# Optimization experiments

Measured on AMD Instinct MI355X. Metric: run time of the kernel, lower is better.

The kernel has to match this reference:

```python
import jax, jax.numpy as jnp
import numpy as np

B, T, E = 2, 4096, 768
H = 12
WIN = 256  # one-sided window w; band width = 2w+1


def setup_inputs() -> dict:
    key = jax.random.key(0)
    k1, k2, k3, k4 = jax.random.split(key, 4)
    scale = 1.0 / np.sqrt(E)
    return {
        "x": jax.random.normal(k1, (B, T, E), dtype=jnp.float32),
        "Wq": jax.random.normal(k2, (E, E), dtype=jnp.float32) * scale,
        "Wk": jax.random.normal(k3, (E, E), dtype=jnp.float32) * scale,
        "Wv": jax.random.normal(k4, (E, E), dtype=jnp.float32) * scale,
    }


def reference(x, Wq, Wk, Wv):
    b, t, e = x.shape
    h, w = H, WIN
    s = e // h
    Wb = 2 * w + 1          # band width
    nc = t // w             # number of query chunks of size w

    # projections (nn.Linear, bias=False): y = x @ W^T
    q = (x @ Wq.T).reshape(b, t, h, s) * (1.0 / np.sqrt(s))
    k = (x @ Wk.T).reshape(b, t, h, s)
    v = (x @ Wv.T).reshape(b, t, h, s)

    # overlapping key/value chunks: chunk c covers absolute keys [c*w - w, c*w + 2w)
    pad = [(0, 0), (w, w), (0, 0), (0, 0)]
    kp = jnp.pad(k, pad).reshape(b, nc + 2, w, h, s)
    k3 = jnp.concatenate([kp[:, :-2], kp[:, 1:-1], kp[:, 2:]], axis=2)  # [b,nc,3w,h,s]
    vp = jnp.pad(v, pad).reshape(b, nc + 2, w, h, s)
    v3 = jnp.concatenate([vp[:, :-2], vp[:, 1:-1], vp[:, 2:]], axis=2)  # [b,nc,3w,h,s]

    qc = q.reshape(b, nc, w, h, s)
    scores = jnp.einsum('bcxhd,bcyhd->bhcxy', qc, k3)  # [b,h,nc,w,3w]

    # extract the banded diagonals: band j <-> key index p + j in the 3w window
    idx = jnp.arange(w)[:, None] + jnp.arange(Wb)[None, :]  # [w, 2w+1], values in [0,3w)
    band = jnp.take_along_axis(scores, idx[None, None, None], axis=-1)  # [b,h,nc,w,2w+1]
    band = band.reshape(b, h, t, Wb).transpose(0, 2, 1, 3)  # [b,t,h,2w+1]

    # mask_invalid_locations: key absolute pos = i + j - w must lie in [0, t)
    key_pos = jnp.arange(t)[:, None] + jnp.arange(Wb)[None, :] - w
    invalid = (key_pos < 0) | (key_pos >= t)
    band = jnp.where(invalid[None, :, None, :], -jnp.inf, band)

    probs = jax.nn.softmax(band.astype(jnp.float32), axis=-1).astype(x.dtype)

    # sliding_chunks_matmul_pv: scatter band probs back to the 3w window layout
    pc = probs.transpose(0, 2, 1, 3).reshape(b, h, nc, w, Wb)
    pc_pad = jnp.pad(pc, [(0, 0)] * 4 + [(w - 1, w - 1)])  # last axis len 4w-1
    # full[p, m] = band[p, m - p] for m-p in [0, 2w], else 0
    idx2 = (jnp.arange(3 * w)[None, :] - jnp.arange(w)[:, None]) + (w - 1)  # [w, 3w]
    pfull = jnp.take_along_axis(pc_pad, idx2[None, None, None], axis=-1)  # [b,h,nc,w,3w]

    out = jnp.einsum('bhcpm,bcmhd->bcphd', pfull, v3).reshape(b, t, e)
    return out
```

## Files before the change

kernel.cpp:

```cpp
#include <hip/hip_runtime.h>

#define B_ 2
#define T_ 4096
#define E_ 768
#define H_ 12
#define S_ 64
#define WIN_ 256
#define GX_ 32
#define TP_ 4128

typedef unsigned short u16;
typedef unsigned int u32;
typedef __attribute__((ext_vector_type(8))) short bf16x8;
typedef __attribute__((ext_vector_type(4))) short bf16x4;
typedef __attribute__((ext_vector_type(4))) float f32x4;

__device__ __forceinline__ u16 f2bf(float f) {
  u32 u = __float_as_uint(f);
  u += ((u >> 16) & 1u) + 0x7fffu;
  return (u16)(u >> 16);
}

__device__ __forceinline__ u32 cvt_pk_bf16(float lo, float hi) {
  u32 r;
  asm("v_cvt_pk_bf16_f32 %0, %1, %2" : "=v"(r) : "v"(lo), "v"(hi));
  return r;
}

__device__ __forceinline__ void async_copy16(const u16* g, u16* l) {
  __builtin_amdgcn_global_load_lds(
      (const __attribute__((address_space(1))) void*)g,
      (__attribute__((address_space(3))) void*)l, 16, 0, 0);
}

__global__ void cvt_all(const float* __restrict__ x, const float* __restrict__ wq,
                        const float* __restrict__ wk, const float* __restrict__ wv,
                        u16* __restrict__ xb, u16* __restrict__ wb) {
  const int n4x = B_ * T_ * E_ / 4;
  const int n4w = E_ * E_ / 4;
  int i = blockIdx.x * 256 + threadIdx.x;
  const float* src;
  u16* dst;
  int j;
  if (i < n4x) {
    src = x; dst = xb; j = i;
  } else {
    int t = i - n4x;
    int z = t / n4w;
    if (z >= 3) return;
    j = t - z * n4w;
    src = (z == 0) ? wq : ((z == 1) ? wk : wv);
    dst = wb + (size_t)z * E_ * E_;
  }
  float4 v = ((const float4*)src)[j];
  ushort4 o;
  o.x = f2bf(v.x); o.y = f2bf(v.y); o.z = f2bf(v.z); o.w = f2bf(v.w);
  ((ushort4*)dst)[j] = o;
}

__global__ __launch_bounds__(256)
void gemm_qkv(const u16* __restrict__ xb, const u16* __restrict__ wb,
              u16* __restrict__ qkv) {
  const int M = B_ * T_;
  __shared__ u16 As[3][128][32];
  __shared__ u16 Bs[3][128][32];
  int tid = threadIdx.x;
  int lane = tid & 63, wave = tid >> 6;
  int wr = wave >> 1, wc = wave & 1;
  int q8 = lane >> 4, nl = lane & 15;
  int bm = blockIdx.x * 128, bn = blockIdx.y * 128;
  int z = blockIdx.z;
  const u16* A = xb;
  const u16* Bmat = wb + (size_t)z * E_ * E_;
  u16* C = qkv + (size_t)z * M * E_;
  float scale = (z == 0) ? (0.125f * 1.44269504088896f) : 1.0f;

  int r0 = tid >> 2, c0 = tid & 3;
  int cs = c0 ^ (r0 & 3);
  const u16* ga0 = A + (size_t)(bm + r0) * E_ + cs * 8;
  const u16* ga1 = A + (size_t)(bm + r0 + 64) * E_ + cs * 8;
  const u16* gb0 = Bmat + (size_t)(bn + r0) * E_ + cs * 8;
  const u16* gb1 = Bmat + (size_t)(bn + r0 + 64) * E_ + cs * 8;
  int l0 = tid * 8;
  int l1 = tid * 8 + 2048;

  int swz8 = (q8 ^ (nl & 3)) * 8;

  const int NK = E_ / 32;
#pragma unroll
  for (int p = 0; p < 2; ++p) {
    int koff = p * 32;
    async_copy16(ga0 + koff, &As[p][0][0] + l0);
    async_copy16(ga1 + koff, &As[p][0][0] + l1);
    async_copy16(gb0 + koff, &Bs[p][0][0] + l0);
    async_copy16(gb1 + koff, &Bs[p][0][0] + l1);
  }

  f32x4 acc[4][4] = {};

#define KSTEP(KI, BUF, PBUF)                                                   \
  {                                                                            \
    asm volatile("s_waitcnt vmcnt(4) lgkmcnt(0)" ::: "memory");                \
    __builtin_amdgcn_s_barrier();                                              \
    __builtin_amdgcn_sched_barrier(0);                                         \
    int kp = ((KI) + 2 < NK) ? (KI) + 2 : NK - 1;                              \
    int koff = kp * 32;                                                        \
    async_copy16(ga0 + koff, &As[PBUF][0][0] + l0);                            \
    async_copy16(ga1 + koff, &As[PBUF][0][0] + l1);                            \
    async_copy16(gb0 + koff, &Bs[PBUF][0][0] + l0);                            \
    async_copy16(gb1 + koff, &Bs[PBUF][0][0] + l1);                            \
    bf16x8 af[4], bfr[4];                                                      \
    _Pragma("unroll")                                                          \
    for (int i = 0; i < 4; ++i)                                                \
      af[i] = *(const bf16x8*)&As[BUF][wr * 64 + i * 16 + nl][swz8];           \
    _Pragma("unroll")                                                          \
    for (int i = 0; i < 4; ++i)                                                \
      bfr[i] = *(const bf16x8*)&Bs[BUF][wc * 64 + i * 16 + nl][swz8];          \
    __builtin_amdgcn_s_setprio(1);                                             \
    _Pragma("unroll")                                                          \
    for (int i = 0; i < 4; ++i)                                                \
      _Pragma("unroll")                                                        \
      for (int j2 = 0; j2 < 4; ++j2)                                           \
        acc[i][j2] = __builtin_amdgcn_mfma_f32_16x16x32_bf16(af[i], bfr[j2],   \
                                                             acc[i][j2], 0, 0, 0); \
    __builtin_amdgcn_s_setprio(0);                                             \
  }

  for (int kb = 0; kb < NK; kb += 3) {
    KSTEP(kb + 0, 0, 2)
    KSTEP(kb + 1, 1, 0)
    KSTEP(kb + 2, 2, 1)
  }
#undef KSTEP

#pragma unroll
  for (int i = 0; i < 4; ++i)
#pragma unroll
    for (int j2 = 0; j2 < 4; ++j2)
#pragma unroll
      for (int r = 0; r < 4; ++r) {
        int row = bm + wr * 64 + i * 16 + q8 * 4 + r;
        int col = bn + wc * 64 + j2 * 16 + nl;
        C[(size_t)row * E_ + col] = f2bf(acc[i][j2][r] * scale);
      }
}

__global__ void transpose_v(const u16* __restrict__ v, u16* __restrict__ vT) {
  __shared__ u16 lt[64][66];
  int t = threadIdx.x;
  int t0 = blockIdx.x * 64;
  int e0 = blockIdx.y * 64;
  int b = blockIdx.z;
#pragma unroll
  for (int i = 0; i < 2; ++i) {
    int u = t + i * 256;
    int tok = u >> 3, cg = u & 7;
    bf16x8 val = *(const bf16x8*)(v + (size_t)(b * T_ + t0 + tok) * E_ + e0 + cg * 8);
#pragma unroll
    for (int j = 0; j < 8; ++j) lt[tok][cg * 8 + j] = (u16)val[j];
  }
  __syncthreads();
#pragma unroll
  for (int i = 0; i < 2; ++i) {
    int u = t + i * 256;
    int d = u >> 3, ck = u & 7;
    bf16x8 o;
#pragma unroll
    for (int j = 0; j < 8; ++j) o[j] = (short)lt[ck * 8 + j][d];
    *(bf16x8*)(vT + (size_t)(b * E_ + e0 + d) * TP_ + t0 + ck * 8) = o;
  }
}

__global__ __launch_bounds__(256)
void attn_kernel(const u16* __restrict__ qkv, const u16* __restrict__ vT,
                 float* __restrict__ out) {
  const int Mtot = B_ * T_;
  const u16* qb = qkv;
  const u16* kb = qkv + (size_t)Mtot * E_;

  int tid = threadIdx.x;
  int lane = tid & 63, wave = tid >> 6;
  int q8 = lane >> 4, nl = lane & 15;

  int d = blockIdx.y * GX_ + blockIdx.x;
  int xcd = d & 7, jj = d >> 3;
  int nx = xcd * 4 + (jj & 3);
  int ny = jj >> 2;
  int qs = nx * 128;
  int b = ny / H_, h = ny % H_;
  int qw = qs + wave * 32;
  size_t ho = (size_t)h * S_;

  bf16x8 aq[2][2];
#pragma unroll
  for (int mt = 0; mt < 2; ++mt) {
    const u16* qrow = qb + (size_t)(b * T_ + qw + mt * 16 + nl) * E_ + ho;
    aq[mt][0] = *(const bf16x8*)(qrow + q8 * 8);
    aq[mt][1] = *(const bf16x8*)(qrow + 32 + q8 * 8);
  }

  f32x4 O[2][4] = {};
  float lacc[2] = {0.f, 0.f};

  int klo = qw - WIN_; if (klo < 0) klo = 0;
  int khi = qw + 32 + WIN_; if (khi > T_) khi = T_;

  const u16* kbase = kb + (size_t)b * T_ * E_ + ho;
  const u16* vbase = vT + ((size_t)b * E_ + ho) * TP_;

  int alo = ((((q8 << 1) & 3) << 4) + nl) << 2;
  int ahi = alo + 64;
  bool hint = q8 >= 2;

  bf16x8 bk[2][2];
#pragma unroll
  for (int nt = 0; nt < 2; ++nt) {
    const u16* krow = kbase + (size_t)(klo + nt * 16 + nl) * E_;
    bk[nt][0] = *(const bf16x8*)(krow + q8 * 8);
    bk[nt][1] = *(const bf16x8*)(krow + 32 + q8 * 8);
  }

  for (int kt = klo; kt < khi; kt += 32) {
    bf16x8 bv[4];
#pragma unroll
    for (int dt = 0; dt < 4; ++dt)
      bv[dt] = *(const bf16x8*)(vbase + (size_t)(dt * 16 + nl) * TP_ + kt + q8 * 8);

    int ktn = (kt + 32 < khi) ? kt + 32 : kt;
    bf16x8 nbk[2][2];
#pragma unroll
    for (int nt = 0; nt < 2; ++nt) {
      const u16* krow = kbase + (size_t)(ktn + nt * 16 + nl) * E_;
      nbk[nt][0] = *(const bf16x8*)(krow + q8 * 8);
      nbk[nt][1] = *(const bf16x8*)(krow + 32 + q8 * 8);
    }

    f32x4 sc[2][2] = {};
    __builtin_amdgcn_s_setprio(1);
#pragma unroll
    for (int nt = 0; nt < 2; ++nt)
#pragma unroll
      for (int mt = 0; mt < 2; ++mt) {
        sc[mt][nt] = __builtin_amdgcn_mfma_f32_16x16x32_bf16(bk[nt][0], aq[mt][0], sc[mt][nt], 0, 0, 0);
        sc[mt][nt] = __builtin_amdgcn_mfma_f32_16x16x32_bf16(bk[nt][1], aq[mt][1], sc[mt][nt], 0, 0, 0);
      }
    __builtin_amdgcn_s_setprio(0);

    if (kt < qw - 225 || kt > qw + 225) {
#pragma unroll
      for (int mt = 0; mt < 2; ++mt)
#pragma unroll
        for (int nt = 0; nt < 2; ++nt)
#pragma unroll
          for (int r = 0; r < 4; ++r) {
            int qa = qw + mt * 16 + nl;
            int ka = kt + nt * 16 + q8 * 4 + r;
            int dd = ka - qa;
            sc[mt][nt][r] = (dd < -WIN_ || dd > WIN_) ? -1e30f : sc[mt][nt][r];
          }
    }

#pragma unroll
    for (int mt = 0; mt < 2; ++mt) {
      float s = 0.f;
#pragma unroll
      for (int nt = 0; nt < 2; ++nt)
#pragma unroll
        for (int r = 0; r < 4; ++r) {
          float p = exp2f(sc[mt][nt][r]);
          sc[mt][nt][r] = p;
          s += p;
        }
      lacc[mt] += s;
    }

    bf16x8 ap[2];
#pragma unroll
    for (int mt = 0; mt < 2; ++mt) {
      u32 pk00 = cvt_pk_bf16(sc[mt][0][0], sc[mt][0][1]);
      u32 pk01 = cvt_pk_bf16(sc[mt][0][2], sc[mt][0][3]);
      u32 pk10 = cvt_pk_bf16(sc[mt][1][0], sc[mt][1][1]);
      u32 pk11 = cvt_pk_bf16(sc[mt][1][2], sc[mt][1][3]);
      int q0a = __builtin_amdgcn_ds_bpermute(alo, (int)pk00);
      int q0b = __builtin_amdgcn_ds_bpermute(alo, (int)pk10);
      int q1a = __builtin_amdgcn_ds_bpermute(alo, (int)pk01);
      int q1b = __builtin_amdgcn_ds_bpermute(alo, (int)pk11);
      int q2a = __builtin_amdgcn_ds_bpermute(ahi, (int)pk00);
      int q2b = __builtin_amdgcn_ds_bpermute(ahi, (int)pk10);
      int q3a = __builtin_amdgcn_ds_bpermute(ahi, (int)pk01);
      int q3b = __builtin_amdgcn_ds_bpermute(ahi, (int)pk11);
      union { u32 w[4]; bf16x8 v; } u;
      u.w[0] = (u32)(hint ? q0b : q0a);
      u.w[1] = (u32)(hint ? q1b : q1a);
      u.w[2] = (u32)(hint ? q2b : q2a);
      u.w[3] = (u32)(hint ? q3b : q3a);
      ap[mt] = u.v;
    }

    __builtin_amdgcn_s_setprio(1);
#pragma unroll
    for (int dt = 0; dt < 4; ++dt)
#pragma unroll
      for (int mt = 0; mt < 2; ++mt)
        O[mt][dt] = __builtin_amdgcn_mfma_f32_16x16x32_bf16(ap[mt], bv[dt], O[mt][dt], 0, 0, 0);
    __builtin_amdgcn_s_setprio(0);

#pragma unroll
    for (int nt = 0; nt < 2; ++nt) {
      bk[nt][0] = nbk[nt][0];
      bk[nt][1] = nbk[nt][1];
    }
  }

#pragma unroll
  for (int mt = 0; mt < 2; ++mt) {
    lacc[mt] += __shfl_xor(lacc[mt], 16);
    lacc[mt] += __shfl_xor(lacc[mt], 32);
  }

#pragma unroll
  for (int mt = 0; mt < 2; ++mt)
#pragma unroll
    for (int r = 0; r < 4; ++r) {
      float lq = __shfl(lacc[mt], (lane & 48) | (q8 * 4 + r));
      float inv = 1.0f / lq;
      int qa = qw + mt * 16 + q8 * 4 + r;
      float* op = out + (size_t)(b * T_ + qa) * E_ + ho;
#pragma unroll
      for (int dt = 0; dt < 4; ++dt)
        op[dt * 16 + nl] = O[mt][dt][r] * inv;
    }
}

extern "C" void kernel_launch(void* const* d_in, const int* in_sizes, int n_in,
                              void* d_out, int out_size, void* d_ws, size_t ws_size,
                              hipStream_t stream) {
  const float* x  = (const float*)d_in[0];
  const float* Wq = (const float*)d_in[1];
  const float* Wk = (const float*)d_in[2];
  const float* Wv = (const float*)d_in[3];
  float* out = (float*)d_out;

  const size_t M = (size_t)B_ * T_;
  u16* xb  = (u16*)d_ws;
  u16* wb  = xb + M * E_;
  u16* qkv = wb + 3 * (size_t)E_ * E_;
  u16* vT  = xb;

  const int n4x = B_ * T_ * E_ / 4;
  const int n4w = E_ * E_ / 4;
  int cvt_blocks = (n4x + 3 * n4w + 255) / 256;
  cvt_all<<<cvt_blocks, 256, 0, stream>>>(x, Wq, Wk, Wv, xb, wb);

  dim3 g1(M / 128, E_ / 128, 3);
  gemm_qkv<<<g1, 256, 0, stream>>>(xb, wb, qkv);

  dim3 gt(T_ / 64, E_ / 64, B_);
  transpose_v<<<gt, 256, 0, stream>>>(qkv + 2 * M * E_, vT);

  dim3 g2(GX_, B_ * H_);
  attn_kernel<<<g2, 256, 0, stream>>>(qkv, vT, out);
}
```

Baseline: 176.6 us.

## Switch QKV GEMM to double-buffered 64-wide K tiles

```diff
diff --git a/kernel.cpp b/kernel.cpp
--- a/kernel.cpp
+++ b/kernel.cpp
@@ -62,8 +62,8 @@
 void gemm_qkv(const u16* __restrict__ xb, const u16* __restrict__ wb,
               u16* __restrict__ qkv) {
   const int M = B_ * T_;
-  __shared__ u16 As[3][128][32];
-  __shared__ u16 Bs[3][128][32];
+  __shared__ u16 As[2][128][64];
+  __shared__ u16 Bs[2][128][64];
   int tid = threadIdx.x;
   int lane = tid & 63, wave = tid >> 6;
   int wr = wave >> 1, wc = wave & 1;
@@ -75,61 +75,63 @@
   u16* C = qkv + (size_t)z * M * E_;
   float scale = (z == 0) ? (0.125f * 1.44269504088896f) : 1.0f;
 
-  int r0 = tid >> 2, c0 = tid & 3;
-  int cs = c0 ^ (r0 & 3);
-  const u16* ga0 = A + (size_t)(bm + r0) * E_ + cs * 8;
-  const u16* ga1 = A + (size_t)(bm + r0 + 64) * E_ + cs * 8;
-  const u16* gb0 = Bmat + (size_t)(bn + r0) * E_ + cs * 8;
-  const u16* gb1 = Bmat + (size_t)(bn + r0 + 64) * E_ + cs * 8;
-  int l0 = tid * 8;
-  int l1 = tid * 8 + 2048;
-
-  int swz8 = (q8 ^ (nl & 3)) * 8;
-
-  const int NK = E_ / 32;
-#pragma unroll
-  for (int p = 0; p < 2; ++p) {
-    int koff = p * 32;
-    async_copy16(ga0 + koff, &As[p][0][0] + l0);
-    async_copy16(ga1 + koff, &As[p][0][0] + l1);
-    async_copy16(gb0 + koff, &Bs[p][0][0] + l0);
-    async_copy16(gb1 + koff, &Bs[p][0][0] + l1);
+  int r0 = tid >> 3, c0 = tid & 7;
+  int cs = c0 ^ (r0 & 7);
+  const u16* ga = A + (size_t)(bm + r0) * E_ + cs * 8;
+  const u16* gb = Bmat + (size_t)(bn + r0) * E_ + cs * 8;
+  int ld = tid * 8;
+
+  int sw0 = (q8 ^ (nl & 7)) * 8;
+
+  const int NK = E_ / 64;
+#pragma unroll
+  for (int m = 0; m < 4; ++m) {
+    async_copy16(ga + (size_t)(32 * m) * E_, &As[0][0][0] + ld + m * 2048);
+    async_copy16(gb + (size_t)(32 * m) * E_, &Bs[0][0][0] + ld + m * 2048);
   }
 
   f32x4 acc[4][4] = {};
 
-#define KSTEP(KI, BUF, PBUF)                                                   \
+#define KSTEP(KI, BUF, NBUF)                                                   \
   {                                                                            \
-    asm volatile("s_waitcnt vmcnt(4) lgkmcnt(0)" ::: "memory");                \
+    asm volatile("s_waitcnt lgkmcnt(0)" ::: "memory");                         \
     __builtin_amdgcn_s_barrier();                                              \
     __builtin_amdgcn_sched_barrier(0);                                         \
-    int kp = ((KI) + 2 < NK) ? (KI) + 2 : NK - 1;                              \
-    int koff = kp * 32;                                                        \
-    async_copy16(ga0 + koff, &As[PBUF][0][0] + l0);                            \
-    async_copy16(ga1 + koff, &As[PBUF][0][0] + l1);                            \
-    async_copy16(gb0 + koff, &Bs[PBUF][0][0] + l0);                            \
-    async_copy16(gb1 + koff, &Bs[PBUF][0][0] + l1);                            \
-    bf16x8 af[4], bfr[4];                                                      \
+    int kp = ((KI) + 1 < NK) ? (KI) + 1 : NK - 1;                              \
+    int koff = kp * 64;                                                        \
     _Pragma("unroll")                                                          \
-    for (int i = 0; i < 4; ++i)                                                \
-      af[i] = *(const bf16x8*)&As[BUF][wr * 64 + i * 16 + nl][swz8];           \
+    for (int m = 0; m < 4; ++m) {                                              \
+      async_copy16(ga + (size_t)(32 * m) * E_ + koff,                          \
+                   &As[NBUF][0][0] + ld + m * 2048);                           \
+      async_copy16(gb + (size_t)(32 * m) * E_ + koff,                          \
+                   &Bs[NBUF][0][0] + ld + m * 2048);                           \
+    }                                                                          \
+    asm volatile("s_waitcnt vmcnt(8) lgkmcnt(0)" ::: "memory");                \
+    __builtin_amdgcn_sched_barrier(0);                                         \
     _Pragma("unroll")                                                          \
-    for (int i = 0; i < 4; ++i)                                                \
-      bfr[i] = *(const bf16x8*)&Bs[BUF][wc * 64 + i * 16 + nl][swz8];          \
-    __builtin_amdgcn_s_setprio(1);                                             \
-    _Pragma("unroll")                                                          \
-    for (int i = 0; i < 4; ++i)                                                \
+    for (int kk = 0; kk < 2; ++kk) {                                           \
+      bf16x8 af[4], bfr[4];                                                    \
+      int sw = sw0 ^ (kk * 32);                                                \
       _Pragma("unroll")                                                        \
-      for (int j2 = 0; j2 < 4; ++j2)                                           \
-        acc[i][j2] = __builtin_amdgcn_mfma_f32_16x16x32_bf16(af[i], bfr[j2],   \
-                                                             acc[i][j2], 0, 0, 0); \
-    __builtin_amdgcn_s_setprio(0);                                             \
-  }
-
-  for (int kb = 0; kb < NK; kb += 3) {
-    KSTEP(kb + 0, 0, 2)
+      for (int i = 0; i < 4; ++i)                                              \
+        af[i] = *(const bf16x8*)&As[BUF][wr * 64 + i * 16 + nl][sw];           \
+      _Pragma("unroll")                                                        \
+      for (int i = 0; i < 4; ++i)                                              \
+        bfr[i] = *(const bf16x8*)&Bs[BUF][wc * 64 + i * 16 + nl][sw];          \
+      __builtin_amdgcn_s_setprio(1);                                           \
+      _Pragma("unroll")                                                        \
+      for (int i = 0; i < 4; ++i)                                              \
+        _Pragma("unroll")                                                      \
+        for (int j2 = 0; j2 < 4; ++j2)                                         \
+          acc[i][j2] = __builtin_amdgcn_mfma_f32_16x16x32_bf16(af[i], bfr[j2], \
+                                                               acc[i][j2], 0, 0, 0); \
+      __builtin_amdgcn_s_setprio(0);                                           \
+    }                                                                          \
+  }
+
+  for (int kb = 0; kb < NK; kb += 2) {
+    KSTEP(kb + 0, 0, 1)
     KSTEP(kb + 1, 1, 0)
-    KSTEP(kb + 2, 2, 1)
   }
 #undef KSTEP
 
```

After: 177.6 us. No clear change (+0.5%).
